# Optimization experiments

Measured on AMD Instinct MI355X. Metric: run time of the kernel, lower is better.

Reference implementation:

```python
import jax, jax.numpy as jnp
import numpy as np

TOP_K = 2

def _mlp(x, w_gate_up, b_gate_up, w_down):
    # x: [T,H]; w_gate_up: [2I,H]; b_gate_up: [2I]; w_down: [H,I]
    gu = x @ w_gate_up.T + b_gate_up
    i = w_gate_up.shape[0] // 2
    h = jax.nn.silu(gu[..., :i]) * gu[..., i:]  # SiluAndMul
    return h @ w_down.T

def setup_inputs() -> dict:
    key = jax.random.key(0)
    ks = jax.random.split(key, 8)
    T, H, I, E = 8192, 1024, 512, 16
    s = 0.02  # weight init scale
    return {
        "hidden_states": jax.random.normal(ks[0], (T, H), jnp.float32),
        "gate_w": jax.random.normal(ks[1], (E, H), jnp.float32) * s,
        "w_gate_up": jax.random.normal(ks[2], (E, 2 * I, H), jnp.float32) * s,
        "b_gate_up": jax.random.normal(ks[3], (E, 2 * I), jnp.float32) * s,
        "w_down": jax.random.normal(ks[4], (E, H, I), jnp.float32) * s,
        "ws_gate_up": jax.random.normal(ks[5], (2 * I, H), jnp.float32) * s,
        "bs_gate_up": jax.random.normal(ks[6], (2 * I,), jnp.float32) * s,
        "ws_down": jax.random.normal(ks[7], (H, I), jnp.float32) * s,
    }

def reference(hidden_states, gate_w, w_gate_up, b_gate_up, w_down,
              ws_gate_up, bs_gate_up, ws_down):
    x = hidden_states  # [T,H]
    E = gate_w.shape[0]

    # shared expert
    shared_out = _mlp(x, ws_gate_up, bs_gate_up, ws_down)  # [T,H]

    # router: softmax in float32, then top-k and renormalize (norm_topk_prob)
    router_logits = x @ gate_w.T  # [T,E]
    probs = jax.nn.softmax(router_logits.astype(jnp.float32), axis=-1)
    rw, sel = jax.lax.top_k(probs, TOP_K)  # [T,K]
    rw = rw / jnp.sum(rw, axis=-1, keepdims=True)

    # per-token per-expert weight [T,E] (0 for unselected experts)
    ew = jnp.sum(jax.nn.one_hot(sel, E, dtype=rw.dtype) * rw[..., None], axis=1)

    # dense all-experts MLP (faithful to the naive masked loop, vectorized)
    gu = jnp.einsum('th,eih->eti', x, w_gate_up) + b_gate_up[:, None, :]  # [E,T,2I]
    I = gu.shape[-1] // 2
    act = jax.nn.silu(gu[..., :I]) * gu[..., I:]  # [E,T,I]
    # scaling by routing weight commutes with the linear down_proj
    wact = act * ew.T[:, :, None].astype(act.dtype)  # [E,T,I]
    final = jnp.einsum('eti,ehi->th', wact, w_down)  # [T,H]

    return final + shared_out
```

## Files before the change

kernel.cpp:

```cpp
#include <hip/hip_runtime.h>
#include <hip/hip_bf16.h>
#include <cstdint>
#include <cstddef>

typedef _Float16 f16;
typedef _Float16 f16x4 __attribute__((ext_vector_type(4)));
typedef _Float16 f16x8 __attribute__((ext_vector_type(8)));
typedef float f32x4 __attribute__((ext_vector_type(4)));

#define GPTR(p) ((const __attribute__((address_space(1))) void*)(p))
#define LPTR(p) ((__attribute__((address_space(3))) void*)(p))

#define T_TOK 8192
#define H_DIM 1024
#define I_DIM 512
#define N_EXP 16
#define N_ALL 17
#define TOPK 2
#define NSLOT (T_TOK * TOPK)
#define NSLOT_ALL (NSLOT + T_TOK)

#define MAX_TILES 208
#define XCD_TILES (MAX_TILES / 8)

__device__ __forceinline__ void cast8(const float* __restrict__ src, f16* __restrict__ dst, int c) {
    float4 a = ((const float4*)src)[(size_t)c * 2];
    float4 b = ((const float4*)src)[(size_t)c * 2 + 1];
    f16x8 o = { (f16)a.x, (f16)a.y, (f16)a.z, (f16)a.w,
                (f16)b.x, (f16)b.y, (f16)b.z, (f16)b.w };
    *(f16x8*)(dst + (size_t)c * 8) = o;
}
__device__ __forceinline__ void split8(const float* __restrict__ src,
                                       f16* __restrict__ h, f16* __restrict__ l, int c) {
    float4 a = ((const float4*)src)[(size_t)c * 2];
    float4 b = ((const float4*)src)[(size_t)c * 2 + 1];
    float v[8] = { a.x, a.y, a.z, a.w, b.x, b.y, b.z, b.w };
    f16x8 hh, ll;
#pragma unroll
    for (int r = 0; r < 8; r++) { hh[r] = (f16)v[r]; ll[r] = (f16)(v[r] - (float)hh[r]); }
    *(f16x8*)(h + (size_t)c * 8) = hh;
    *(f16x8*)(l + (size_t)c * 8) = ll;
}
__device__ __forceinline__ void cpy8(const float* __restrict__ s, float* __restrict__ d, int c) {
    ((float4*)d)[(size_t)c * 2]     = ((const float4*)s)[(size_t)c * 2];
    ((float4*)d)[(size_t)c * 2 + 1] = ((const float4*)s)[(size_t)c * 2 + 1];
}

#define PREP_BLOCKS 2048
__global__ __launch_bounds__(256) void prep_kernel(
    const float* __restrict__ x, const float* __restrict__ gw,
    const float* __restrict__ wgu, const float* __restrict__ wsgu,
    const float* __restrict__ wd, const float* __restrict__ wsd,
    const float* __restrict__ bgu, const float* __restrict__ bsgu,
    f16* __restrict__ x_h, f16* __restrict__ x_l,
    f16* __restrict__ gw_h, f16* __restrict__ gw_l,
    f16* __restrict__ wguA, f16* __restrict__ wdA,
    float* __restrict__ biasA, int* __restrict__ counts) {
    constexpr int C_X   = 1048576;
    constexpr int C_GW  = 2048;
    constexpr int C_WGU = 2097152;
    constexpr int C_WSG = 131072;
    constexpr int C_WD  = 1048576;
    constexpr int C_WSD = 65536;
    constexpr int C_BG  = 2048;
    constexpr int C_BS  = 128;
    constexpr int NTOT  = C_X + C_GW + C_WGU + C_WSG + C_WD + C_WSD + C_BG + C_BS + 1;
    const int stride = gridDim.x * blockDim.x;
    for (int i = blockIdx.x * blockDim.x + threadIdx.x; i < NTOT; i += stride) {
        int r = i;
        if (r < C_X)  { split8(x, x_h, x_l, r); continue; }  r -= C_X;
        if (r < C_GW) { split8(gw, gw_h, gw_l, r); continue; } r -= C_GW;
        if (r < C_WGU){ cast8(wgu, wguA, r); continue; }      r -= C_WGU;
        if (r < C_WSG){ cast8(wsgu, wguA + (size_t)16 * 1024 * 1024, r); continue; } r -= C_WSG;
        if (r < C_WD) { cast8(wd, wdA, r); continue; }        r -= C_WD;
        if (r < C_WSD){ cast8(wsd, wdA + (size_t)16 * 1024 * 512, r); continue; }    r -= C_WSD;
        if (r < C_BG) { cpy8(bgu, biasA, r); continue; }      r -= C_BG;
        if (r < C_BS) { cpy8(bsgu, biasA + 16384, r); continue; } r -= C_BS;
        ((int4*)counts)[0] = (int4){0,0,0,0};
        ((int4*)counts)[1] = (int4){0,0,0,0};
        ((int4*)counts)[2] = (int4){0,0,0,0};
        ((int4*)counts)[3] = (int4){0,0,0,0};
    }
}

__global__ __launch_bounds__(256) void logits_kernel(
    const f16* __restrict__ Xh, const f16* __restrict__ Xl,
    const f16* __restrict__ Gh, const f16* __restrict__ Gl,
    float* __restrict__ L) {
    const int wave = threadIdx.x >> 6, lane = threadIdx.x & 63;
    const int m0 = blockIdx.x * 64 + wave * 16;
    const int qm = lane & 15, quad = lane >> 4;
    const size_t arow = (size_t)(m0 + qm) * H_DIM + quad * 8;
    const size_t brow = (size_t)qm * H_DIM + quad * 8;
    f32x4 acc = (f32x4){0.f, 0.f, 0.f, 0.f};
    const f16* ap;
    const f16* bp;
    ap = Xh + arow; bp = Gh + brow;
#pragma unroll 8
    for (int k0 = 0; k0 < H_DIM; k0 += 32) {
        acc = __builtin_amdgcn_mfma_f32_16x16x32_f16(*(const f16x8*)ap, *(const f16x8*)bp, acc, 0, 0, 0);
        ap += 32; bp += 32;
    }
    ap = Xh + arow; bp = Gl + brow;
#pragma unroll 8
    for (int k0 = 0; k0 < H_DIM; k0 += 32) {
        acc = __builtin_amdgcn_mfma_f32_16x16x32_f16(*(const f16x8*)ap, *(const f16x8*)bp, acc, 0, 0, 0);
        ap += 32; bp += 32;
    }
    ap = Xl + arow; bp = Gh + brow;
#pragma unroll 8
    for (int k0 = 0; k0 < H_DIM; k0 += 32) {
        acc = __builtin_amdgcn_mfma_f32_16x16x32_f16(*(const f16x8*)ap, *(const f16x8*)bp, acc, 0, 0, 0);
        ap += 32; bp += 32;
    }
#pragma unroll
    for (int r = 0; r < 4; r++)
        L[(size_t)(m0 + quad * 4 + r) * N_EXP + qm] = acc[r];
}

__global__ void topk_kernel(const float* __restrict__ L, int* __restrict__ sel,
                            float* __restrict__ rw, int* __restrict__ counts) {
    __shared__ int lc[N_EXP];
    const int tid = threadIdx.x;
    if (tid < N_EXP) lc[tid] = 0;
    __syncthreads();
    const int t = blockIdx.x * 256 + tid;
    float lg[16];
    const float4* lp = (const float4*)(L + (size_t)t * N_EXP);
#pragma unroll
    for (int q = 0; q < 4; q++) {
        float4 v = lp[q];
        lg[q * 4 + 0] = v.x; lg[q * 4 + 1] = v.y; lg[q * 4 + 2] = v.z; lg[q * 4 + 3] = v.w;
    }
    float best = -1e30f, sec = -1e30f; int bi = 0, si = 0;
#pragma unroll
    for (int j = 0; j < 16; j++) {
        float lj = lg[j];
        if (lj > best) { sec = best; si = bi; best = lj; bi = j; }
        else if (lj > sec) { sec = lj; si = j; }
    }
    float w1 = 1.f / (1.f + __expf(sec - best));
    sel[t * 2] = bi; sel[t * 2 + 1] = si;
    rw[t * 2] = w1;  rw[t * 2 + 1] = 1.f - w1;
    atomicAdd(&lc[bi], 1);
    atomicAdd(&lc[si], 1);
    __syncthreads();
    if (tid < N_EXP) atomicAdd(&counts[tid], lc[tid]);
}

__global__ void prefix_kernel(const int* __restrict__ counts, int* __restrict__ offsets,
                              int* __restrict__ cursors, int* __restrict__ tiles) {
    __shared__ int ts[17];
    __shared__ int cnt[16];
    const int tid = threadIdx.x;
    if (tid == 0) {
        int s = 0, t = 64;
        for (int e = 0; e < 16; e++) {
            int c = counts[e];
            cnt[e] = c;
            offsets[e] = s; cursors[e] = s; s += c;
            ts[e] = t; t += (c + 127) >> 7;
        }
        offsets[16] = s;
        offsets[17] = s + T_TOK;
        ts[16] = t;
    }
    __syncthreads();
    const int ntot = ts[16];
    if (tid < 16) {
        int t0 = ts[tid], M = cnt[tid];
        for (int m0 = 0, k = 0; m0 < M; m0 += 128, k++) tiles[t0 + k] = (tid << 20) | m0;
    } else if (tid == 16) {
        for (int k = 0; k < 64; k++) tiles[k] = (16 << 20) | (k * 128);
    }
    for (int j = ntot + tid; j < MAX_TILES; j += 64) tiles[j] = -1;
}

__global__ void scatter_kernel(const int* __restrict__ sel, const float* __restrict__ rw,
                               int* __restrict__ cursors, int* __restrict__ btok,
                               float* __restrict__ bw, int* __restrict__ pos) {
    int t = blockIdx.x * blockDim.x + threadIdx.x;
    if (t >= T_TOK) return;
#pragma unroll
    for (int k = 0; k < TOPK; k++) {
        int e = sel[t * 2 + k];
        int p = atomicAdd(&cursors[e], 1);
        btok[p] = t;
        bw[p] = rw[t * 2 + k];
        pos[t * 2 + k] = p;
    }
    btok[NSLOT + t] = t;
    bw[NSLOT + t] = 1.f;
}

__device__ __forceinline__ void xcd_tile_map(int g, int& ti, int& n0i) {
    const int x = g & 7;
    const int q = g >> 3;
    ti  = x * XCD_TILES + (q >> 3);
    n0i = q & 7;
}

#define WAITV4_BAR() do { \
    asm volatile("s_waitcnt vmcnt(4)" ::: "memory"); \
    __builtin_amdgcn_s_barrier(); } while (0)
#define WAITV0_BAR() do { \
    asm volatile("s_waitcnt vmcnt(0)" ::: "memory"); \
    __builtin_amdgcn_s_barrier(); } while (0)

__global__ __launch_bounds__(256, 4) void gemm_gateup_act(
    const f16* __restrict__ X,
    const f16* __restrict__ W,
    const float* __restrict__ bias,
    const float* __restrict__ bw,
    f16* __restrict__ ACT,
    const int* __restrict__ offsets,
    const int* __restrict__ btok,
    const int* __restrict__ tiles) {
    constexpr int K = H_DIM;
    constexpr int NT = K / 32;
    int ti, n0i;
    xcd_tile_map(blockIdx.x, ti, n0i);
    const int td = tiles[ti];
    if (td < 0) return;
    const int e  = td >> 20;
    const int m0 = td & 0xFFFFF;
    const int n0 = n0i * 64;
    const int base = offsets[e];
    const int M = offsets[e + 1] - base;

    const f16* Wb   = W + (size_t)e * 1024 * K;
    const float* bb = bias + (size_t)e * 1024;

    __shared__ f16 As[2][128 * 32];
    __shared__ f16 Bg[2][64 * 32];
    __shared__ f16 Bu[2][64 * 32];

    const int tid  = threadIdx.x;
    const int wave = tid >> 6;
    const int lane = tid & 63;
    const int srow = lane >> 2;
    const int csw  = ((lane & 3) ^ ((srow >> 1) & 3)) * 8;

    int ar0 = m0 + wave * 32 + srow;
    int ar1 = ar0 + 16;
    int r0 = min(ar0, M - 1), r1 = min(ar1, M - 1);
    const f16* ap0 = X + (size_t)btok[base + r0] * K + csw;
    const f16* ap1 = X + (size_t)btok[base + r1] * K + csw;
    const int brow = n0 + wave * 16 + srow;
    const f16* bg0 = Wb + (size_t)brow * K + csw;
    const f16* bu0 = bg0 + (size_t)512 * K;
    f16* la0 = &As[0][(wave * 32) * 32];
    f16* la1 = la0 + 16 * 32;
    f16* lg0 = &Bg[0][(wave * 16) * 32];
    f16* lu0 = &Bu[0][(wave * 16) * 32];
    constexpr int AST = 128 * 32;
    constexpr int BST = 64 * 32;

    const int wm = (wave >> 1) * 64;
    const int wn = (wave & 1) * 32;
    const int qm = lane & 15;
    const int quad = lane >> 4;
    const int qsw = (quad ^ ((qm >> 1) & 3)) * 8;

    f32x4 accg[4][2], accu[4][2];
#pragma unroll
    for (int i = 0; i < 4; i++)
#pragma unroll
        for (int j = 0; j < 2; j++) {
            accg[i][j] = (f32x4){0.f, 0.f, 0.f, 0.f};
            accu[i][j] = (f32x4){0.f, 0.f, 0.f, 0.f};
        }

#define GU_STAGE(b) do { \
    __builtin_amdgcn_global_load_lds(GPTR(ap0), LPTR(la0 + (b) * AST), 16, 0, 0); \
    __builtin_amdgcn_global_load_lds(GPTR(ap1), LPTR(la1 + (b) * AST), 16, 0, 0); \
    __builtin_amdgcn_global_load_lds(GPTR(bg0), LPTR(lg0 + (b) * BST), 16, 0, 0); \
    __builtin_amdgcn_global_load_lds(GPTR(bu0), LPTR(lu0 + (b) * BST), 16, 0, 0); \
    ap0 += 32; ap1 += 32; bg0 += 32; bu0 += 32; } while (0)

#define GU_COMPUTE(b) do { \
    f16x8 af[4], gf[2], uf[2]; \
    _Pragma("unroll") \
    for (int i = 0; i < 4; i++) af[i] = *(const f16x8*)&As[b][(wm + i * 16 + qm) * 32 + qsw]; \
    _Pragma("unroll") \
    for (int j = 0; j < 2; j++) { \
        gf[j] = *(const f16x8*)&Bg[b][(wn + j * 16 + qm) * 32 + qsw]; \
        uf[j] = *(const f16x8*)&Bu[b][(wn + j * 16 + qm) * 32 + qsw]; \
    } \
    _Pragma("unroll") \
    for (int i = 0; i < 4; i++) \
        _Pragma("unroll") \
        for (int j = 0; j < 2; j++) { \
            accg[i][j] = __builtin_amdgcn_mfma_f32_16x16x32_f16(af[i], gf[j], accg[i][j], 0, 0, 0); \
            accu[i][j] = __builtin_amdgcn_mfma_f32_16x16x32_f16(af[i], uf[j], accu[i][j], 0, 0, 0); \
        } } while (0)

    GU_STAGE(0);
    for (int t = 0; t < NT; t += 2) {
        __builtin_amdgcn_s_barrier();
        GU_STAGE(1);
        WAITV4_BAR();
        GU_COMPUTE(0);
        __builtin_amdgcn_s_barrier();
        if (t + 2 < NT) {
            GU_STAGE(0);
            WAITV4_BAR();
        } else {
            WAITV0_BAR();
        }
        GU_COMPUTE(1);
    }

#pragma unroll
    for (int i = 0; i < 4; i++) {
#pragma unroll
        for (int j = 0; j < 2; j++) {
            const int colg = n0 + wn + j * 16 + qm;
            const float bvg = bb[colg];
            const float bvu = bb[colg + 512];
#pragma unroll
            for (int r = 0; r < 4; r++) {
                const int lr = wm + i * 16 + quad * 4 + r;
                const int m = m0 + lr;
                if (m < M) {
                    float g = accg[i][j][r] + bvg;
                    float u = accu[i][j][r] + bvu;
                    float sl = g / (1.f + __expf(-g));
                    ACT[(size_t)(base + m) * 512 + colg] = (f16)(sl * u * bw[base + m]);
                }
            }
        }
    }
}

__global__ __launch_bounds__(256, 4) void gemm_down(
    const f16* __restrict__ ACT,
    const f16* __restrict__ W,
    f16* __restrict__ DOWN,
    const int* __restrict__ offsets,
    const int* __restrict__ tiles) {
    constexpr int K = I_DIM;
    constexpr int NT = K / 32;
    int ti, n0i;
    xcd_tile_map(blockIdx.x, ti, n0i);
    const int td = tiles[ti];
    if (td < 0) return;
    const int e  = td >> 20;
    const int m0 = td & 0xFFFFF;
    const int n0 = n0i * 128;
    const int base = offsets[e];
    const int M = offsets[e + 1] - base;

    const f16* Wb = W + (size_t)e * 1024 * K;

    __shared__ f16 As[2][128 * 32];
    __shared__ f16 Bs[2][128 * 32];

    const int tid  = threadIdx.x;
    const int wave = tid >> 6;
    const int lane = tid & 63;
    const int srow = lane >> 2;
    const int csw  = ((lane & 3) ^ ((srow >> 1) & 3)) * 8;

    int ar0 = m0 + wave * 32 + srow;
    int ar1 = ar0 + 16;
    int r0 = min(ar0, M - 1), r1 = min(ar1, M - 1);
    const f16* ap0 = ACT + (size_t)(base + r0) * K + csw;
    const f16* ap1 = ACT + (size_t)(base + r1) * K + csw;
    const f16* bp0 = Wb + (size_t)(n0 + wave * 32 + srow) * K + csw;
    const f16* bp1 = bp0 + (size_t)16 * K;
    f16* la0 = &As[0][(wave * 32) * 32];  f16* la1 = la0 + 16 * 32;
    f16* lb0 = &Bs[0][(wave * 32) * 32];  f16* lb1 = lb0 + 16 * 32;
    constexpr int DST = 128 * 32;

    const int wm = (wave >> 1) * 64;
    const int wn = (wave & 1) * 64;
    const int qm = lane & 15;
    const int quad = lane >> 4;
    const int qsw = (quad ^ ((qm >> 1) & 3)) * 8;

    f32x4 acc[4][4];
#pragma unroll
    for (int i = 0; i < 4; i++)
#pragma unroll
        for (int j = 0; j < 4; j++) acc[i][j] = (f32x4){0.f, 0.f, 0.f, 0.f};

#define DN_STAGE(b) do { \
    __builtin_amdgcn_global_load_lds(GPTR(ap0), LPTR(la0 + (b) * DST), 16, 0, 0); \
    __builtin_amdgcn_global_load_lds(GPTR(ap1), LPTR(la1 + (b) * DST), 16, 0, 0); \
    __builtin_amdgcn_global_load_lds(GPTR(bp0), LPTR(lb0 + (b) * DST), 16, 0, 0); \
    __builtin_amdgcn_global_load_lds(GPTR(bp1), LPTR(lb1 + (b) * DST), 16, 0, 0); \
    ap0 += 32; ap1 += 32; bp0 += 32; bp1 += 32; } while (0)

#define DN_COMPUTE(b) do { \
    f16x8 af[4], bfr[4]; \
    _Pragma("unroll") \
    for (int i = 0; i < 4; i++) af[i]  = *(const f16x8*)&As[b][(wm + i * 16 + qm) * 32 + qsw]; \
    _Pragma("unroll") \
    for (int j = 0; j < 4; j++) bfr[j] = *(const f16x8*)&Bs[b][(wn + j * 16 + qm) * 32 + qsw]; \
    _Pragma("unroll") \
    for (int i = 0; i < 4; i++) \
        _Pragma("unroll") \
        for (int j = 0; j < 4; j++) \
            acc[i][j] = __builtin_amdgcn_mfma_f32_16x16x32_f16(af[i], bfr[j], acc[i][j], 0, 0, 0); \
    } while (0)

    DN_STAGE(0);
    for (int t = 0; t < NT; t += 2) {
        __builtin_amdgcn_s_barrier();
        DN_STAGE(1);
        WAITV4_BAR();
        DN_COMPUTE(0);
        __builtin_amdgcn_s_barrier();
        if (t + 2 < NT) {
            DN_STAGE(0);
            WAITV4_BAR();
        } else {
            WAITV0_BAR();
        }
        DN_COMPUTE(1);
    }

#pragma unroll
    for (int i = 0; i < 4; i++) {
#pragma unroll
        for (int j = 0; j < 4; j++) {
            const int col = n0 + wn + j * 16 + qm;
#pragma unroll
            for (int r = 0; r < 4; r++) {
                const int lr = wm + i * 16 + quad * 4 + r;
                const int m = m0 + lr;
                if (m < M) DOWN[(size_t)(base + m) * 1024 + col] = (f16)acc[i][j][r];
            }
        }
    }
}

__global__ void combine_kernel(const f16* __restrict__ DOWN, const int* __restrict__ pos,
                               float* __restrict__ OUT) {
    int idx = blockIdx.x * blockDim.x + threadIdx.x;
    int t = idx >> 7;
    int c = (idx & 127) * 8;
    int p1 = pos[t * 2], p2 = pos[t * 2 + 1];
    f16x8 a = *(const f16x8*)(DOWN + (size_t)(NSLOT + t) * 1024 + c);
    f16x8 b = *(const f16x8*)(DOWN + (size_t)p1 * 1024 + c);
    f16x8 d = *(const f16x8*)(DOWN + (size_t)p2 * 1024 + c);
    float4 o0, o1;
    o0.x = (float)a[0] + (float)b[0] + (float)d[0];
    o0.y = (float)a[1] + (float)b[1] + (float)d[1];
    o0.z = (float)a[2] + (float)b[2] + (float)d[2];
    o0.w = (float)a[3] + (float)b[3] + (float)d[3];
    o1.x = (float)a[4] + (float)b[4] + (float)d[4];
    o1.y = (float)a[5] + (float)b[5] + (float)d[5];
    o1.z = (float)a[6] + (float)b[6] + (float)d[6];
    o1.w = (float)a[7] + (float)b[7] + (float)d[7];
    *(float4*)(OUT + (size_t)t * 1024 + c) = o0;
    *(float4*)(OUT + (size_t)t * 1024 + c + 4) = o1;
}

extern "C" void kernel_launch(void* const* d_in, const int* in_sizes, int n_in,
                              void* d_out, int out_size, void* d_ws, size_t ws_size,
                              hipStream_t stream) {
    const float* x    = (const float*)d_in[0];
    const float* gw   = (const float*)d_in[1];
    const float* wgu  = (const float*)d_in[2];
    const float* bgu  = (const float*)d_in[3];
    const float* wd   = (const float*)d_in[4];
    const float* wsgu = (const float*)d_in[5];
    const float* bsgu = (const float*)d_in[6];
    const float* wsd  = (const float*)d_in[7];
    float* out = (float*)d_out;

    char* ws = (char*)d_ws;
    size_t off = 0;
    auto take = [&](size_t b) { char* p = ws + off; off = (off + b + 255) & ~(size_t)255; return p; };
    f16* x_h    = (f16*)take((size_t)T_TOK * H_DIM * 2);
    f16* x_l    = (f16*)take((size_t)T_TOK * H_DIM * 2);
    f16* gw_h   = (f16*)take((size_t)N_EXP * H_DIM * 2);
    f16* gw_l   = (f16*)take((size_t)N_EXP * H_DIM * 2);
    f16* wguA   = (f16*)take((size_t)N_ALL * 1024 * H_DIM * 2);
    f16* wdA    = (f16*)take((size_t)N_ALL * 1024 * I_DIM * 2);
    float* biasA = (float*)take((size_t)N_ALL * 1024 * 4);
    f16* act    = (f16*)take((size_t)NSLOT_ALL * I_DIM * 2);
    f16* down   = (f16*)take((size_t)NSLOT_ALL * 1024 * 2);
    float* logits = (float*)take((size_t)T_TOK * N_EXP * 4);
    int*   sel    = (int*)take((size_t)NSLOT * 4);
    float* rw     = (float*)take((size_t)NSLOT * 4);
    int*   btok   = (int*)take((size_t)NSLOT_ALL * 4);
    float* bw     = (float*)take((size_t)NSLOT_ALL * 4);
    int*   pos    = (int*)take((size_t)NSLOT * 4);
    int*   counts = (int*)take(64);
    int*   offs   = (int*)take(128);
    int*   curs   = (int*)take(64);
    int*   tiles  = (int*)take(MAX_TILES * 4);

    prep_kernel<<<PREP_BLOCKS, 256, 0, stream>>>(x, gw, wgu, wsgu, wd, wsd, bgu, bsgu,
                                                 x_h, x_l, gw_h, gw_l, wguA, wdA, biasA, counts);

    logits_kernel<<<T_TOK / 64, 256, 0, stream>>>(x_h, x_l, gw_h, gw_l, logits);
    topk_kernel<<<T_TOK / 256, 256, 0, stream>>>(logits, sel, rw, counts);
    prefix_kernel<<<1, 64, 0, stream>>>(counts, offs, curs, tiles);
    scatter_kernel<<<T_TOK / 256, 256, 0, stream>>>(sel, rw, curs, btok, bw, pos);

    gemm_gateup_act<<<dim3(MAX_TILES * 8, 1, 1), 256, 0, stream>>>(x_h, wguA, biasA, bw, act, offs, btok, tiles);

    gemm_down<<<dim3(MAX_TILES * 8, 1, 1), 256, 0, stream>>>(act, wdA, down, offs, tiles);

    combine_kernel<<<T_TOK * 1024 / 8 / 256, 256, 0, stream>>>(down, pos, out);
}
```

Before: 386.3 us.

## Triple-buffer LDS in gate-up and down GEMMs with one barrier per k-step

Both expert GEMM kernels move from double-buffered to triple-buffered shared-memory staging. Each k-step now waits on the load issued two steps earlier, issues the next async global-to-LDS load, and computes, so there is a single barrier per step instead of two. The aim is to hide more load latency and cut barrier overhead. The cost is 50% more LDS per block, which may limit occupancy under the 4-blocks-per-CU launch bound, and the loop bounds are now hardcoded for K=1024 and K=512.

```diff
diff --git a/kernel.cpp b/kernel.cpp
--- a/kernel.cpp
+++ b/kernel.cpp
@@ -200,10 +200,10 @@
     n0i = q & 7;
 }
 
-#define WAITV4_BAR() do { \
+#define VW4_BAR() do { \
     asm volatile("s_waitcnt vmcnt(4)" ::: "memory"); \
     __builtin_amdgcn_s_barrier(); } while (0)
-#define WAITV0_BAR() do { \
+#define VW0_BAR() do { \
     asm volatile("s_waitcnt vmcnt(0)" ::: "memory"); \
     __builtin_amdgcn_s_barrier(); } while (0)
 
@@ -217,7 +217,6 @@
     const int* __restrict__ btok,
     const int* __restrict__ tiles) {
     constexpr int K = H_DIM;
-    constexpr int NT = K / 32;
     int ti, n0i;
     xcd_tile_map(blockIdx.x, ti, n0i);
     const int td = tiles[ti];
@@ -231,9 +230,9 @@
     const f16* Wb   = W + (size_t)e * 1024 * K;
     const float* bb = bias + (size_t)e * 1024;
 
-    __shared__ f16 As[2][128 * 32];
-    __shared__ f16 Bg[2][64 * 32];
-    __shared__ f16 Bu[2][64 * 32];
+    __shared__ f16 As[3][128 * 32];
+    __shared__ f16 Bg[3][64 * 32];
+    __shared__ f16 Bu[3][64 * 32];
 
     const int tid  = threadIdx.x;
     const int wave = tid >> 6;
@@ -295,21 +294,17 @@
             accu[i][j] = __builtin_amdgcn_mfma_f32_16x16x32_f16(af[i], uf[j], accu[i][j], 0, 0, 0); \
         } } while (0)
 
+#define GU_STEP(bc, bs) do { VW4_BAR(); GU_STAGE(bs); GU_COMPUTE(bc); } while (0)
+
     GU_STAGE(0);
-    for (int t = 0; t < NT; t += 2) {
-        __builtin_amdgcn_s_barrier();
-        GU_STAGE(1);
-        WAITV4_BAR();
-        GU_COMPUTE(0);
-        __builtin_amdgcn_s_barrier();
-        if (t + 2 < NT) {
-            GU_STAGE(0);
-            WAITV4_BAR();
-        } else {
-            WAITV0_BAR();
-        }
-        GU_COMPUTE(1);
-    }
+    GU_STAGE(1);
+    for (int t = 0; t < 30; t += 3) {
+        GU_STEP(0, 2);
+        GU_STEP(1, 0);
+        GU_STEP(2, 1);
+    }
+    VW4_BAR(); GU_COMPUTE(0);
+    VW0_BAR(); GU_COMPUTE(1);
 
 #pragma unroll
     for (int i = 0; i < 4; i++) {
@@ -340,7 +335,6 @@
     const int* __restrict__ offsets,
     const int* __restrict__ tiles) {
     constexpr int K = I_DIM;
-    constexpr int NT = K / 32;
     int ti, n0i;
     xcd_tile_map(blockIdx.x, ti, n0i);
     const int td = tiles[ti];
@@ -353,8 +347,8 @@
 
     const f16* Wb = W + (size_t)e * 1024 * K;
 
-    __shared__ f16 As[2][128 * 32];
-    __shared__ f16 Bs[2][128 * 32];
+    __shared__ f16 As[3][128 * 32];
+    __shared__ f16 Bs[3][128 * 32];
 
     const int tid  = threadIdx.x;
     const int wave = tid >> 6;
@@ -405,21 +399,19 @@
             acc[i][j] = __builtin_amdgcn_mfma_f32_16x16x32_f16(af[i], bfr[j], acc[i][j], 0, 0, 0); \
     } while (0)
 
+#define DN_STEP(bc, bs) do { VW4_BAR(); DN_STAGE(bs); DN_COMPUTE(bc); } while (0)
+
     DN_STAGE(0);
-    for (int t = 0; t < NT; t += 2) {
-        __builtin_amdgcn_s_barrier();
-        DN_STAGE(1);
-        WAITV4_BAR();
-        DN_COMPUTE(0);
-        __builtin_amdgcn_s_barrier();
-        if (t + 2 < NT) {
-            DN_STAGE(0);
-            WAITV4_BAR();
-        } else {
-            WAITV0_BAR();
-        }
-        DN_COMPUTE(1);
-    }
+    DN_STAGE(1);
+    for (int t = 0; t < 12; t += 3) {
+        DN_STEP(0, 2);
+        DN_STEP(1, 0);
+        DN_STEP(2, 1);
+    }
+    DN_STEP(0, 2);
+    DN_STEP(1, 0);
+    VW4_BAR(); DN_COMPUTE(2);
+    VW0_BAR(); DN_COMPUTE(0);
 
 #pragma unroll
     for (int i = 0; i < 4; i++) {
```

New measurement: 430.4 us. +11.4%, slower.
